# Kernel optimization log

Measured on AMD Instinct MI355X. Metric: run time of the kernel, lower is better.

Reference implementation:

```python
import jax, jax.numpy as jnp
import numpy as np

INPUT_NC = 512
N_HEADS = 16
D_KEY = 64
SCALE = D_KEY ** 0.5


def setup_inputs() -> dict:
    key = jax.random.key(0)
    k1, k2, k3, k4, k5, k6 = jax.random.split(key, 6)
    bs, d_seq = 8, 1024
    v = jax.random.normal(k1, (bs, d_seq, INPUT_NC), dtype=jnp.float32)
    # key-padding mask, True = masked out; broadcast over heads and query dim
    pad_mask = jax.random.bernoulli(k2, 0.1, (bs, 1, 1, d_seq))
    # fc1: input_nc -> 2*n_heads*d_key (fused K,Q projection)
    W1 = jax.random.normal(k3, (INPUT_NC, 2 * N_HEADS * D_KEY), dtype=jnp.float32) * (1.0 / np.sqrt(INPUT_NC))
    b1 = jax.random.normal(k4, (2 * N_HEADS * D_KEY,), dtype=jnp.float32) * 0.01
    # fc2: n_heads*input_nc -> input_nc
    W2 = jax.random.normal(k5, (N_HEADS * INPUT_NC, INPUT_NC), dtype=jnp.float32) * (1.0 / np.sqrt(N_HEADS * INPUT_NC))
    b2 = jax.random.normal(k6, (INPUT_NC,), dtype=jnp.float32) * 0.01
    return {"v": v, "pad_mask": pad_mask, "W1": W1, "b1": b1, "W2": W2, "b2": b2}


def reference(v, pad_mask, W1, b1, W2, b2):
    bs, d_seq, nc = v.shape
    # fused KQ projection: [bs, S, 2*H*dk] -> [bs, H, S, 2*dk]
    kq = (v @ W1 + b1).reshape(bs, d_seq, N_HEADS, 2 * D_KEY).transpose(0, 2, 1, 3)
    k, q = kq[..., :D_KEY], kq[..., D_KEY:]  # chunk: k first, q second
    attn = jnp.einsum('bhqd,bhkd->bhqk', q, k) / SCALE
    attn = jnp.where(pad_mask, jnp.float32(-1000.0), attn)
    attn = jax.nn.softmax(attn, axis=3)
    # AV with unprojected v broadcast across heads: [bs, H, S, nc]
    out = jnp.einsum('bhqk,bkc->bhqc', attn, v)
    out = out.transpose(0, 2, 1, 3).reshape(bs, d_seq, N_HEADS * nc)
    out = out @ W2 + b2
    return (out, attn)
```

## Files before the change

### kernel.cpp

```cpp
#include <hip/hip_runtime.h>


typedef __attribute__((ext_vector_type(8))) short bf16x8;
typedef __attribute__((ext_vector_type(4))) float f32x4;
typedef __attribute__((ext_vector_type(4))) unsigned short u16x4;

__device__ __forceinline__ unsigned short f2bf(float f) {
  unsigned u = __builtin_bit_cast(unsigned, f);
  u += 0x7FFFu + ((u >> 16) & 1u);
  return (unsigned short)(u >> 16);
}
__device__ __forceinline__ float bf2f(unsigned short u) {
  return __builtin_bit_cast(float, (unsigned)u << 16);
}

__device__ __forceinline__ void gload_lds16(const unsigned short* g, unsigned short* l) {
  __builtin_amdgcn_global_load_lds(
      (const __attribute__((address_space(1))) unsigned int*)(g),
      (__attribute__((address_space(3))) unsigned int*)(l), 16, 0, 0);
}


__global__ void transpose_cvt_kernel(const float* __restrict__ in,
                                     unsigned short* __restrict__ out,
                                     int R, int C) {
  __shared__ float tile[32][33];
  int c0 = blockIdx.x * 32, r0 = blockIdx.y * 32;
  int tx = threadIdx.x & 31, ty = threadIdx.x >> 5;
#pragma unroll
  for (int i = ty; i < 32; i += 8)
    tile[i][tx] = in[(size_t)(r0 + i) * C + (c0 + tx)];
  __syncthreads();
#pragma unroll
  for (int i = ty; i < 32; i += 8)
    out[(size_t)(c0 + i) * R + (r0 + tx)] = f2bf(tile[tx][i]);
}

__global__ void prep_v_kernel(const float* __restrict__ v,
                              unsigned short* __restrict__ vbf,
                              unsigned short* __restrict__ vt) {
  __shared__ float tile[32][33];
  int c0 = blockIdx.x * 32, r0 = blockIdx.y * 32;
  int tx = threadIdx.x & 31, ty = threadIdx.x >> 5;
#pragma unroll
  for (int i = ty; i < 32; i += 8) {
    float val = v[(size_t)(r0 + i) * 512 + (c0 + tx)];
    tile[i][tx] = val;
    vbf[(size_t)(r0 + i) * 512 + (c0 + tx)] = f2bf(val);
  }
  __syncthreads();
#pragma unroll
  for (int i = ty; i < 32; i += 8)
    vt[(size_t)(c0 + i) * 8192 + (r0 + tx)] = f2bf(tile[tx][i]);
}

__launch_bounds__(256)
__global__ void gemm1_kernel(const unsigned short* __restrict__ vbf,
                             const unsigned short* __restrict__ w1t,
                             const float* __restrict__ b1,
                             unsigned short* __restrict__ q_ws,
                             unsigned short* __restrict__ k_ws) {
  const int m0 = blockIdx.y * 128, n0 = blockIdx.x * 128;
  const int w = threadIdx.x >> 6, l = threadIdx.x & 63;
  const int wr = w >> 1, wc = w & 1, lr = l & 15, lg = l >> 4;
  f32x4 acc[4][4];
#pragma unroll
  for (int mi = 0; mi < 4; ++mi)
#pragma unroll
    for (int ni = 0; ni < 4; ++ni) acc[mi][ni] = (f32x4){0.f, 0.f, 0.f, 0.f};

  for (int k0 = 0; k0 < 512; k0 += 32) {
    bf16x8 a[4], bb[4];
#pragma unroll
    for (int mi = 0; mi < 4; ++mi)
      a[mi] = *reinterpret_cast<const bf16x8*>(
          vbf + (size_t)(m0 + wr * 64 + mi * 16 + lr) * 512 + k0 + lg * 8);
#pragma unroll
    for (int ni = 0; ni < 4; ++ni)
      bb[ni] = *reinterpret_cast<const bf16x8*>(
          w1t + (size_t)(n0 + wc * 64 + ni * 16 + lr) * 512 + k0 + lg * 8);
#pragma unroll
    for (int mi = 0; mi < 4; ++mi)
#pragma unroll
      for (int ni = 0; ni < 4; ++ni)
        acc[mi][ni] = __builtin_amdgcn_mfma_f32_16x16x32_bf16(a[mi], bb[ni], acc[mi][ni], 0, 0, 0);
  }
#pragma unroll
  for (int mi = 0; mi < 4; ++mi)
#pragma unroll
    for (int ni = 0; ni < 4; ++ni) {
      int col = n0 + wc * 64 + ni * 16 + lr;
      int h = col >> 7, j = col & 127;
      float bias = b1[col];
#pragma unroll
      for (int r = 0; r < 4; ++r) {
        int row = m0 + wr * 64 + mi * 16 + lg * 4 + r;
        int bb_ = row >> 10, s = row & 1023;
        unsigned short bv = f2bf(acc[mi][ni][r] + bias);
        size_t base = ((size_t)(bb_ * 16 + h) << 16) + (size_t)s * 64;
        if (j < 64) k_ws[base + j] = bv;
        else        q_ws[base + j - 64] = bv;
      }
    }
}

__launch_bounds__(512)
__global__ void scores_kernel(const unsigned short* __restrict__ q_ws,
                              const unsigned short* __restrict__ k_ws,
                              const int* __restrict__ pad,
                              float* __restrict__ attn_out,
                              unsigned short* __restrict__ eb,
                              float* __restrict__ linv_ws) {
  const int wg = (blockIdx.x & 7) * 512 + (blockIdx.x >> 3);
  const int qt = wg & 31, h = (wg >> 5) & 15, b = wg >> 9;
  const int bh = b * 16 + h, q0 = qt * 32;
  const int w = threadIdx.x >> 6, l = threadIdx.x & 63;
  const int lr = l & 15, lg = l >> 4;

  __shared__ unsigned short E_lds[32][1032];
  __shared__ float lw[8][32];
  __shared__ float linv_s[32];

  const unsigned short* qb = q_ws + ((size_t)bh << 16);
  const unsigned short* kb = k_ws + ((size_t)bh << 16);
  const int* pmb = pad + b * 1024;

  bf16x8 a_q[2][2];
#pragma unroll
  for (int mf = 0; mf < 2; ++mf)
#pragma unroll
    for (int ks = 0; ks < 2; ++ks)
      a_q[mf][ks] = *reinterpret_cast<const bf16x8*>(
          qb + (size_t)(q0 + mf * 16 + lr) * 64 + ks * 32 + lg * 8);

  float l_run[2][4];
#pragma unroll
  for (int mf = 0; mf < 2; ++mf)
#pragma unroll
    for (int r = 0; r < 4; ++r) l_run[mf][r] = 0.f;

#pragma unroll
  for (int sub = 0; sub < 2; ++sub) {
    const int c0 = w * 128 + sub * 64;
    f32x4 s[2][4];
#pragma unroll
    for (int mf = 0; mf < 2; ++mf)
#pragma unroll
      for (int nf = 0; nf < 4; ++nf) s[mf][nf] = (f32x4){0.f, 0.f, 0.f, 0.f};
#pragma unroll
    for (int ks = 0; ks < 2; ++ks) {
      bf16x8 bk[4];
#pragma unroll
      for (int nf = 0; nf < 4; ++nf)
        bk[nf] = *reinterpret_cast<const bf16x8*>(
            kb + (size_t)(c0 + nf * 16 + lr) * 64 + ks * 32 + lg * 8);
#pragma unroll
      for (int mf = 0; mf < 2; ++mf)
#pragma unroll
        for (int nf = 0; nf < 4; ++nf)
          s[mf][nf] = __builtin_amdgcn_mfma_f32_16x16x32_bf16(a_q[mf][ks], bk[nf], s[mf][nf], 0, 0, 0);
    }
    int msk[4];
#pragma unroll
    for (int nf = 0; nf < 4; ++nf) msk[nf] = pmb[c0 + nf * 16 + lr];
#pragma unroll
    for (int mf = 0; mf < 2; ++mf)
#pragma unroll
      for (int nf = 0; nf < 4; ++nf)
#pragma unroll
        for (int r = 0; r < 4; ++r) {
          float e = msk[nf] ? 0.f : __expf(s[mf][nf][r] * 0.125f);
          l_run[mf][r] += e;
          E_lds[mf * 16 + lg * 4 + r][c0 + nf * 16 + lr] = f2bf(e);
        }
  }

#pragma unroll
  for (int mf = 0; mf < 2; ++mf)
#pragma unroll
    for (int r = 0; r < 4; ++r) {
      float v = l_run[mf][r];
      v += __shfl_xor(v, 1); v += __shfl_xor(v, 2);
      v += __shfl_xor(v, 4); v += __shfl_xor(v, 8);
      if (lr == 0) lw[w][mf * 16 + lg * 4 + r] = v;
    }
  __syncthreads();
  if (threadIdx.x < 32) {
    float s = 0.f;
#pragma unroll
    for (int ww = 0; ww < 8; ++ww) s += lw[ww][threadIdx.x];
    float li = 1.f / s;
    linv_s[threadIdx.x] = li;
    linv_ws[(size_t)bh * 1024 + q0 + threadIdx.x] = li;
  }
  __syncthreads();

  {
    const int row = threadIdx.x >> 4;
    const int cb = threadIdx.x & 15;
    const float sc = linv_s[row];
    float* rowp = attn_out + ((size_t)bh << 20) + (size_t)(q0 + row) * 1024;
    unsigned short* ebrow = eb + ((size_t)bh << 20) + (size_t)(q0 + row) * 1024;
#pragma unroll
    for (int i = 0; i < 8; ++i) {
      int c8 = cb * 8 + i * 128;
      bf16x8 ev = *reinterpret_cast<const bf16x8*>(&E_lds[row][c8]);
      f32x4 o0, o1;
#pragma unroll
      for (int j = 0; j < 4; ++j) o0[j] = bf2f((unsigned short)ev[j]) * sc;
#pragma unroll
      for (int j = 0; j < 4; ++j) o1[j] = bf2f((unsigned short)ev[4 + j]) * sc;
      *reinterpret_cast<f32x4*>(rowp + c8) = o0;
      *reinterpret_cast<f32x4*>(rowp + c8 + 4) = o1;
      *reinterpret_cast<bf16x8*>(ebrow + c8) = ev;
    }
  }
}

__launch_bounds__(256)
__global__ void pv_kernel(const unsigned short* __restrict__ eb,
                          const unsigned short* __restrict__ vt,
                          const float* __restrict__ linv_ws,
                          unsigned short* __restrict__ o_ws) {
  const int wg = (blockIdx.x & 7) * 512 + (blockIdx.x >> 3);
  const int nt = wg & 3, mt = (wg >> 2) & 7, bh = wg >> 5;
  const int b = bh >> 4, h = bh & 15;
  const int m0 = mt * 128, n0 = nt * 128;

  __shared__ unsigned short Asm[2][128 * 32];
  __shared__ unsigned short Bsm[2][128 * 32];
  const int w = threadIdx.x >> 6, l = threadIdx.x & 63;
  const int wr = w >> 1, wc = w & 1, lr = l & 15, lg = l >> 4;

  f32x4 acc[4][4];
#pragma unroll
  for (int mi = 0; mi < 4; ++mi)
#pragma unroll
    for (int ni = 0; ni < 4; ++ni) acc[mi][ni] = (f32x4){0.f, 0.f, 0.f, 0.f};

  const int srow = threadIdx.x >> 2;
  const int scol = (threadIdx.x & 3) * 8;
  const unsigned short* gA0 = eb + ((size_t)bh << 20) + (size_t)(m0 + srow) * 1024 + scol;
  const unsigned short* gA1 = gA0 + (size_t)64 * 1024;
  const unsigned short* gB0 = vt + (size_t)(n0 + srow) * 8192 + (size_t)b * 1024 + scol;
  const unsigned short* gB1 = gB0 + (size_t)64 * 8192;
  const int ldsoff = w * 512;

  float linv_r[4][4];
  {
    const float* lrow = linv_ws + (size_t)bh * 1024 + m0 + wr * 64 + lg * 4;
#pragma unroll
    for (int mi = 0; mi < 4; ++mi)
#pragma unroll
      for (int r = 0; r < 4; ++r) linv_r[mi][r] = lrow[mi * 16 + r];
  }

  auto STAGE = [&](int buf, int kt) {
    int k0 = kt * 32;
    gload_lds16(gA0 + k0, &Asm[buf][ldsoff]);
    gload_lds16(gA1 + k0, &Asm[buf][64 * 32 + ldsoff]);
    gload_lds16(gB0 + k0, &Bsm[buf][ldsoff]);
    gload_lds16(gB1 + k0, &Bsm[buf][64 * 32 + ldsoff]);
  };
  auto COMPUTE = [&](int buf) {
    bf16x8 a[4], bb[4];
#pragma unroll
    for (int mi = 0; mi < 4; ++mi)
      a[mi] = *reinterpret_cast<const bf16x8*>(&Asm[buf][(wr * 64 + mi * 16 + lr) * 32 + lg * 8]);
#pragma unroll
    for (int ni = 0; ni < 4; ++ni)
      bb[ni] = *reinterpret_cast<const bf16x8*>(&Bsm[buf][(wc * 64 + ni * 16 + lr) * 32 + lg * 8]);
    __builtin_amdgcn_s_setprio(1);
#pragma unroll
    for (int mi = 0; mi < 4; ++mi)
#pragma unroll
      for (int ni = 0; ni < 4; ++ni)
        acc[mi][ni] = __builtin_amdgcn_mfma_f32_16x16x32_bf16(a[mi], bb[ni], acc[mi][ni], 0, 0, 0);
    __builtin_amdgcn_s_setprio(0);
  };

  STAGE(0, 0);
  __syncthreads();
  int cur = 0;
  for (int kt = 0; kt < 31; ++kt) {
    STAGE(cur ^ 1, kt + 1);
    COMPUTE(cur);
    __syncthreads();
    cur ^= 1;
  }
  COMPUTE(cur);

#pragma unroll
  for (int mi = 0; mi < 4; ++mi)
#pragma unroll
    for (int ni = 0; ni < 4; ++ni)
#pragma unroll
      for (int r = 0; r < 4; ++r) {
        int row = m0 + wr * 64 + mi * 16 + lg * 4 + r;
        int col = n0 + wc * 64 + ni * 16 + lr;
        o_ws[(size_t)(b * 1024 + row) * 8192 + h * 512 + col] =
            f2bf(acc[mi][ni][r] * linv_r[mi][r]);
      }
}

__launch_bounds__(256)
__global__ void gemm2_kernel(const unsigned short* __restrict__ o_ws,
                             const unsigned short* __restrict__ w2t,
                             const float* __restrict__ b2,
                             float* __restrict__ y) {
  const int wg = (blockIdx.x & 7) * 64 + (blockIdx.x >> 3);
  const int nt = wg & 3, mt = wg >> 2;
  const int m0 = mt * 64, n0 = nt * 128;

  __shared__ unsigned short As[2][64 * 32];
  __shared__ unsigned short Bs[2][128 * 32];
  const int w = threadIdx.x >> 6, l = threadIdx.x & 63;
  const int wr = w >> 1, wc = w & 1, lr = l & 15, lg = l >> 4;

  f32x4 acc[2][4];
#pragma unroll
  for (int mi = 0; mi < 2; ++mi)
#pragma unroll
    for (int ni = 0; ni < 4; ++ni) acc[mi][ni] = (f32x4){0.f, 0.f, 0.f, 0.f};

  const int srow = threadIdx.x >> 2;
  const int scol = (threadIdx.x & 3) * 8;
  const unsigned short* gA  = o_ws + (size_t)(m0 + srow) * 8192 + scol;
  const unsigned short* gB0 = w2t + (size_t)(n0 + srow) * 8192 + scol;
  const unsigned short* gB1 = gB0 + (size_t)64 * 8192;
  const int ldsoff = w * 512;

  auto STAGE = [&](int buf, int kt) {
    int k0 = kt * 32;
    gload_lds16(gA + k0, &As[buf][ldsoff]);
    gload_lds16(gB0 + k0, &Bs[buf][ldsoff]);
    gload_lds16(gB1 + k0, &Bs[buf][64 * 32 + ldsoff]);
  };

  auto COMPUTE = [&](int buf) {
    bf16x8 a[2], bb[4];
#pragma unroll
    for (int mi = 0; mi < 2; ++mi)
      a[mi] = *reinterpret_cast<const bf16x8*>(&As[buf][(wr * 32 + mi * 16 + lr) * 32 + lg * 8]);
#pragma unroll
    for (int ni = 0; ni < 4; ++ni)
      bb[ni] = *reinterpret_cast<const bf16x8*>(&Bs[buf][(wc * 64 + ni * 16 + lr) * 32 + lg * 8]);
    __builtin_amdgcn_s_setprio(1);
#pragma unroll
    for (int mi = 0; mi < 2; ++mi)
#pragma unroll
      for (int ni = 0; ni < 4; ++ni)
        acc[mi][ni] = __builtin_amdgcn_mfma_f32_16x16x32_bf16(a[mi], bb[ni], acc[mi][ni], 0, 0, 0);
    __builtin_amdgcn_s_setprio(0);
  };

  STAGE(0, 0);
  __syncthreads();
  int cur = 0;
  for (int kt = 0; kt < 255; ++kt) {
    STAGE(cur ^ 1, kt + 1);
    COMPUTE(cur);
    __syncthreads();
    cur ^= 1;
  }
  COMPUTE(cur);

#pragma unroll
  for (int mi = 0; mi < 2; ++mi)
#pragma unroll
    for (int ni = 0; ni < 4; ++ni) {
      int col = n0 + wc * 64 + ni * 16 + lr;
      float bias = b2[col];
#pragma unroll
      for (int r = 0; r < 4; ++r)
        y[(size_t)(m0 + wr * 32 + mi * 16 + lg * 4 + r) * 512 + col] = acc[mi][ni][r] + bias;
    }
}

extern "C" void kernel_launch(void* const* d_in, const int* in_sizes, int n_in,
                              void* d_out, int out_size, void* d_ws, size_t ws_size,
                              hipStream_t stream) {
  const float* v   = (const float*)d_in[0];
  const int*   pad = (const int*)d_in[1];
  const float* W1  = (const float*)d_in[2];
  const float* b1  = (const float*)d_in[3];
  const float* W2  = (const float*)d_in[4];
  const float* b2  = (const float*)d_in[5];
  float* out  = (float*)d_out;
  float* attn = out + (size_t)8 * 1024 * 512;

  char* ws = (char*)d_ws;
  unsigned short* w1t  = (unsigned short*)(ws);
  unsigned short* w2t  = (unsigned short*)(ws + 2097152);
  unsigned short* vt   = (unsigned short*)(ws + 10485760);
  unsigned short* vbf  = (unsigned short*)(ws + 18874368);
  unsigned short* q_ws = (unsigned short*)(ws + 27262976);
  unsigned short* k_ws = (unsigned short*)(ws + 44040192);
  unsigned short* o_ws = (unsigned short*)(ws + 60817408);
  unsigned short* eb   = (unsigned short*)(ws + 195035136);
  float*          linv = (float*)(ws + 463470592);

  transpose_cvt_kernel<<<dim3(64, 16), 256, 0, stream>>>(W1, w1t, 512, 2048);
  transpose_cvt_kernel<<<dim3(16, 256), 256, 0, stream>>>(W2, w2t, 8192, 512);
  prep_v_kernel<<<dim3(16, 256), 256, 0, stream>>>(v, vbf, vt);
  gemm1_kernel<<<dim3(16, 64), 256, 0, stream>>>(vbf, w1t, b1, q_ws, k_ws);
  scores_kernel<<<4096, 512, 0, stream>>>(q_ws, k_ws, pad, attn, eb, linv);
  pv_kernel<<<4096, 256, 0, stream>>>(eb, vt, linv, o_ws);
  gemm2_kernel<<<512, 256, 0, stream>>>(o_ws, w2t, b2, out);
}
```

Before: 686.7 us.

## Triple-buffer PV and output GEMM pipelines with explicit vmcnt waits

Switches the PV and final projection GEMMs from double-buffered LDS staging with full __syncthreads to a three-stage ring buffer. Each stage issues direct global-to-LDS loads two tiles ahead and uses partial s_waitcnt vmcnt plus raw barriers, so one load group can stay in flight during compute. The linv row-scale loads are moved after the main loop to shorten the prologue. This uses more LDS per block, which may lower occupancy, and correctness depends on the hand-counted vmcnt values.

```diff
diff --git a/kernel.cpp b/kernel.cpp
--- a/kernel.cpp
+++ b/kernel.cpp
@@ -19,6 +19,11 @@
       (const __attribute__((address_space(1))) unsigned int*)(g),
       (__attribute__((address_space(3))) unsigned int*)(l), 16, 0, 0);
 }
+
+#define WAITV(N) do { asm volatile("s_waitcnt vmcnt(" #N ")" ::: "memory"); \
+                      __builtin_amdgcn_sched_barrier(0); } while (0)
+#define BAR()    do { __builtin_amdgcn_s_barrier(); \
+                      __builtin_amdgcn_sched_barrier(0); } while (0)
 
 
 __global__ void transpose_cvt_kernel(const float* __restrict__ in,
@@ -227,8 +232,8 @@
   const int b = bh >> 4, h = bh & 15;
   const int m0 = mt * 128, n0 = nt * 128;
 
-  __shared__ unsigned short Asm[2][128 * 32];
-  __shared__ unsigned short Bsm[2][128 * 32];
+  __shared__ unsigned short Asm[3][128 * 32];
+  __shared__ unsigned short Bsm[3][128 * 32];
   const int w = threadIdx.x >> 6, l = threadIdx.x & 63;
   const int wr = w >> 1, wc = w & 1, lr = l & 15, lg = l >> 4;
 
@@ -245,15 +250,6 @@
   const unsigned short* gB0 = vt + (size_t)(n0 + srow) * 8192 + (size_t)b * 1024 + scol;
   const unsigned short* gB1 = gB0 + (size_t)64 * 8192;
   const int ldsoff = w * 512;
-
-  float linv_r[4][4];
-  {
-    const float* lrow = linv_ws + (size_t)bh * 1024 + m0 + wr * 64 + lg * 4;
-#pragma unroll
-    for (int mi = 0; mi < 4; ++mi)
-#pragma unroll
-      for (int r = 0; r < 4; ++r) linv_r[mi][r] = lrow[mi * 16 + r];
-  }
 
   auto STAGE = [&](int buf, int kt) {
     int k0 = kt * 32;
@@ -279,16 +275,28 @@
     __builtin_amdgcn_s_setprio(0);
   };
 
-  STAGE(0, 0);
-  __syncthreads();
+  STAGE(0, 0); STAGE(1, 1); STAGE(2, 2);
   int cur = 0;
-  for (int kt = 0; kt < 31; ++kt) {
-    STAGE(cur ^ 1, kt + 1);
+  for (int kt = 0; kt < 29; ++kt) {
+    WAITV(8);
+    BAR();
     COMPUTE(cur);
-    __syncthreads();
-    cur ^= 1;
-  }
-  COMPUTE(cur);
+    BAR();
+    STAGE(cur, kt + 3);
+    cur = (cur == 2) ? 0 : cur + 1;
+  }
+  WAITV(8); BAR(); COMPUTE(cur); cur = (cur == 2) ? 0 : cur + 1;
+  WAITV(4); BAR(); COMPUTE(cur); cur = (cur == 2) ? 0 : cur + 1;
+  WAITV(0); BAR(); COMPUTE(cur);
+
+  float linv_r[4][4];
+  {
+    const float* lrow = linv_ws + (size_t)bh * 1024 + m0 + wr * 64 + lg * 4;
+#pragma unroll
+    for (int mi = 0; mi < 4; ++mi)
+#pragma unroll
+      for (int r = 0; r < 4; ++r) linv_r[mi][r] = lrow[mi * 16 + r];
+  }
 
 #pragma unroll
   for (int mi = 0; mi < 4; ++mi)
@@ -312,8 +320,8 @@
   const int nt = wg & 3, mt = wg >> 2;
   const int m0 = mt * 64, n0 = nt * 128;
 
-  __shared__ unsigned short As[2][64 * 32];
-  __shared__ unsigned short Bs[2][128 * 32];
+  __shared__ unsigned short As[3][64 * 32];
+  __shared__ unsigned short Bs[3][128 * 32];
   const int w = threadIdx.x >> 6, l = threadIdx.x & 63;
   const int wr = w >> 1, wc = w & 1, lr = l & 15, lg = l >> 4;
 
@@ -354,16 +362,19 @@
     __builtin_amdgcn_s_setprio(0);
   };
 
-  STAGE(0, 0);
-  __syncthreads();
+  STAGE(0, 0); STAGE(1, 1); STAGE(2, 2);
   int cur = 0;
-  for (int kt = 0; kt < 255; ++kt) {
-    STAGE(cur ^ 1, kt + 1);
+  for (int kt = 0; kt < 253; ++kt) {
+    WAITV(6);
+    BAR();
     COMPUTE(cur);
-    __syncthreads();
-    cur ^= 1;
-  }
-  COMPUTE(cur);
+    BAR();
+    STAGE(cur, kt + 3);
+    cur = (cur == 2) ? 0 : cur + 1;
+  }
+  WAITV(6); BAR(); COMPUTE(cur); cur = (cur == 2) ? 0 : cur + 1;
+  WAITV(3); BAR(); COMPUTE(cur); cur = (cur == 2) ? 0 : cur + 1;
+  WAITV(0); BAR(); COMPUTE(cur);
 
 #pragma unroll
   for (int mi = 0; mi < 2; ++mi)
```

Result: no change. 675.2 us (-1.7%).
